# Performance work log

Hardware: AMD Instinct MI355X
Metric: run time of the kernel (lower is better)

Reference implementation:

```python
import jax, jax.numpy as jnp
import numpy as np

D_MODEL = 1024
NUM_HEADS = 16
HEAD_DIM = D_MODEL // NUM_HEADS  # 64
M_BITS = 32
B, N = 4, 2048


def setup_inputs() -> dict:
    key = jax.random.key(0)
    ks = jax.random.split(key, 6)
    s = 1.0 / np.sqrt(D_MODEL)
    se = 1.0 / np.sqrt(HEAD_DIM)
    return {
        "x": jax.random.normal(ks[0], (B, N, D_MODEL), dtype=jnp.float32),
        "Wq": jax.random.normal(ks[1], (D_MODEL, D_MODEL), dtype=jnp.float32) * s,
        "Wk": jax.random.normal(ks[2], (D_MODEL, D_MODEL), dtype=jnp.float32) * s,
        "Wv": jax.random.normal(ks[3], (D_MODEL, D_MODEL), dtype=jnp.float32) * s,
        # per-head witness (bit) encoders: project head_dim -> m_bits
        "W_enc": jax.random.normal(ks[4], (NUM_HEADS, HEAD_DIM, M_BITS), dtype=jnp.float32) * se,
        "Wo": jax.random.normal(ks[5], (D_MODEL, D_MODEL), dtype=jnp.float32) * s,
    }


def reference(x, Wq, Wk, Wv, W_enc, Wo):
    Bsz, Nq, _ = x.shape
    # QKV projections (nn.Linear, no bias): y = x @ W^T
    Q = x @ Wq.T
    K = x @ Wk.T  # self-attention: context = x
    V = x @ Wv.T
    # split heads: [B, N, H, hd]
    Qh = Q.reshape(Bsz, Nq, NUM_HEADS, HEAD_DIM)
    Kh = K.reshape(Bsz, Nq, NUM_HEADS, HEAD_DIM)
    Vh = V.reshape(Bsz, Nq, NUM_HEADS, HEAD_DIM)
    # witness encodings: soft-bit (tanh of random-hyperplane projections), m_bits << head_dim feature space
    q_enc = jnp.tanh(jnp.einsum("bnhd,hdm->bnhm", Qh, W_enc))
    k_enc = jnp.tanh(jnp.einsum("bnhd,hdm->bnhm", Kh, W_enc))
    # witness similarity scores over m_bits instead of full head_dim
    scale = 1.0 / np.sqrt(M_BITS)
    scores = jnp.einsum("bnhm,bkhm->bhnk", q_enc, k_enc) * scale  # [B,H,N,N]
    attn = jax.nn.softmax(scores, axis=-1)
    out = jnp.einsum("bhnk,bkhd->bnhd", attn, Vh).reshape(Bsz, Nq, D_MODEL)
    return out @ Wo.T
```

## Files before the change

### kernel.cpp

```cpp
#include <hip/hip_runtime.h>

typedef unsigned short u16;
typedef unsigned int u32;

typedef __bf16 bfrag __attribute__((ext_vector_type(8)));
typedef float f32x4 __attribute__((ext_vector_type(4)));

__device__ __forceinline__ float b2f(u16 h) {
    u32 u = ((u32)h) << 16;
    return __builtin_bit_cast(float, u);
}
__device__ __forceinline__ u16 f2b(float f) {
    u32 u = __builtin_bit_cast(u32, f);
    u += 0x7fffu + ((u >> 16) & 1u);
    return (u16)(u >> 16);
}
__device__ __forceinline__ u32 packt(float lo, float hi) {
    return (__builtin_bit_cast(u32, lo) >> 16) | (__builtin_bit_cast(u32, hi) & 0xffff0000u);
}

#if defined(__has_builtin)
#if __has_builtin(__builtin_amdgcn_exp2f)
#define EXP2(x) __builtin_amdgcn_exp2f(x)
#endif
#endif
#ifndef EXP2
#define EXP2(x) exp2f(x)
#endif

#if defined(__has_builtin)
#if __has_builtin(__builtin_amdgcn_global_load_lds)
#define HAS_GLL 1
#endif
#endif
#ifndef HAS_GLL
#define HAS_GLL 0
#endif

#if HAS_GLL
typedef __attribute__((address_space(1))) const u32 as1_u32;
typedef __attribute__((address_space(3))) u32 as3_u32;
__device__ __forceinline__ void gl_lds16(const u16* g, u16* l) {
    __builtin_amdgcn_global_load_lds((as1_u32*)g, (as3_u32*)l, 16, 0, 0);
}
#endif

#define BATCH 4
#define SEQ   2048
#define DM    1024
#define NH    16
#define HD    64
#define MB    32
#define STOK  (BATCH * SEQ)
#define QKVW  (3 * DM)

#define QSCALE 0.25503524337503433f
#define TWOLOG2E 2.8853900817779268f

__device__ __forceinline__ void storeC(u16* C, size_t idx, float v)   { C[idx] = f2b(v); }
__device__ __forceinline__ void storeC(float* C, size_t idx, float v) { C[idx] = v; }

__global__ __launch_bounds__(256) void cvt_f32_bf16(
    const float* __restrict__ s, u16* __restrict__ d, int n8)
{
    int i = blockIdx.x * 256 + threadIdx.x;
    if (i >= n8) return;
    const float4* sp = (const float4*)s + (size_t)i * 2;
    float4 a = sp[0], b = sp[1];
    u16 t[8] = { f2b(a.x), f2b(a.y), f2b(a.z), f2b(a.w),
                 f2b(b.x), f2b(b.y), f2b(b.z), f2b(b.w) };
    ((uint4*)d)[i] = *(uint4*)t;
}

__global__ __launch_bounds__(256) void cvt3_f32_bf16(
    const float* __restrict__ a, const float* __restrict__ b,
    const float* __restrict__ c, u16* __restrict__ d, int n8)
{
    const float* s = (blockIdx.y == 0) ? a : ((blockIdx.y == 1) ? b : c);
    u16* dd = d + (size_t)blockIdx.y * n8 * 8;
    int i = blockIdx.x * 256 + threadIdx.x;
    if (i >= n8) return;
    const float4* sp = (const float4*)s + (size_t)i * 2;
    float4 x = sp[0], y = sp[1];
    u16 t[8] = { f2b(x.x), f2b(x.y), f2b(x.z), f2b(x.w),
                 f2b(y.x), f2b(y.y), f2b(y.z), f2b(y.w) };
    ((uint4*)dd)[i] = *(uint4*)t;
}

template <int TBM, typename TC>
__global__ __launch_bounds__(256) void gemm_bt(
    const u16* __restrict__ A, const u16* __restrict__ Bt, TC* __restrict__ C,
    int M, int Nc, int K)
{
    constexpr int FI = TBM / 32;
    __shared__ alignas(16) u16 As[TBM * 32];
    __shared__ alignas(16) u16 Bs[128 * 32];

    const int tid  = threadIdx.x;
    const int wave = tid >> 6;
    const int lane = tid & 63;
    const int quad = lane >> 4;
    const int lrow = lane & 15;
    const int bm = blockIdx.y * TBM;
    const int bn = blockIdx.x * 128;
    const int wm = (wave & 1) * (TBM / 2);
    const int wn = (wave >> 1) * 64;

    f32x4 acc[FI][4] = {};

    for (int k0 = 0; k0 < K; k0 += 32) {
#if HAS_GLL
        for (int p = 0; p < TBM / 64; ++p) {
            int cbase = wave * TBM + p * 64;
            int cme   = cbase + lane;
            int row = cme >> 2, col = (cme & 3) * 8;
            gl_lds16(&A[(size_t)(bm + row) * K + k0 + col], &As[(size_t)cbase * 8]);
        }
        for (int p = 0; p < 2; ++p) {
            int cbase = wave * 128 + p * 64;
            int cme   = cbase + lane;
            int row = cme >> 2, col = (cme & 3) * 8;
            gl_lds16(&Bt[(size_t)(bn + row) * K + k0 + col], &Bs[(size_t)cbase * 8]);
        }
#else
        for (int p = 0; p < TBM / 64; ++p) {
            int idx = p * 256 + tid, row = idx >> 2, col = (idx & 3) * 8;
            *(uint4*)&As[row * 32 + col] = *(const uint4*)&A[(size_t)(bm + row) * K + k0 + col];
        }
        for (int p = 0; p < 2; ++p) {
            int idx = p * 256 + tid, row = idx >> 2, col = (idx & 3) * 8;
            *(uint4*)&Bs[row * 32 + col] = *(const uint4*)&Bt[(size_t)(bn + row) * K + k0 + col];
        }
#endif
        __syncthreads();

        bfrag af[FI], bfv[4];
        for (int i = 0; i < FI; ++i)
            af[i] = *(const bfrag*)&As[(wm + i * 16 + lrow) * 32 + quad * 8];
        for (int j = 0; j < 4; ++j)
            bfv[j] = *(const bfrag*)&Bs[(wn + j * 16 + lrow) * 32 + quad * 8];

        for (int i = 0; i < FI; ++i)
            for (int j = 0; j < 4; ++j)
                acc[i][j] = __builtin_amdgcn_mfma_f32_16x16x32_bf16(af[i], bfv[j], acc[i][j], 0, 0, 0);
        __syncthreads();
    }

    for (int i = 0; i < FI; ++i)
        for (int j = 0; j < 4; ++j)
            for (int r = 0; r < 4; ++r) {
                int row = bm + wm + i * 16 + quad * 4 + r;
                int col = bn + wn + j * 16 + lrow;
                storeC(C, (size_t)row * Nc + col, acc[i][j][r]);
            }
}

__global__ __launch_bounds__(256) void encode_mfma(
    const u16* __restrict__ QKV, const float* __restrict__ Wenc,
    u16* __restrict__ qe, u16* __restrict__ ke)
{
    const int nt = blockIdx.x;
    const int bh = blockIdx.y;
    const int b = bh >> 4, h = bh & 15;
    const int tid = threadIdx.x;
    const int wave = tid >> 6, lane = tid & 63, quad = lane >> 4, lrow = lane & 15;

    __shared__ alignas(16) u16 Wh[32 * 72];
    __shared__ alignas(16) u16 Wl[32 * 72];
    __shared__ alignas(16) u16 Xt[128 * 72];

    for (int p = 0; p < 8; ++p) {
        int d = p * 8 + (tid >> 5);
        int m = tid & 31;
        float w = Wenc[(size_t)h * (HD * MB) + d * MB + m];
        u16 hi = f2b(w);
        u16 lo = f2b(w - b2f(hi));
        Wh[m * 72 + d] = hi;
        Wl[m * 72 + d] = lo;
    }
    __syncthreads();

    bfrag bhf[2][2], blf[2][2];
    for (int n2 = 0; n2 < 2; ++n2)
        for (int kc = 0; kc < 2; ++kc) {
            bhf[n2][kc] = *(const bfrag*)&Wh[(n2 * 16 + lrow) * 72 + kc * 32 + quad * 8];
            blf[n2][kc] = *(const bfrag*)&Wl[(n2 * 16 + lrow) * 72 + kc * 32 + quad * 8];
        }

    const f32x4 zero = {0.f, 0.f, 0.f, 0.f};
    for (int src = 0; src < 2; ++src) {
        __syncthreads();
        const u16* base = QKV + (size_t)(b * SEQ + nt * 128) * QKVW + src * DM + h * HD;
        for (int p = 0; p < 4; ++p) {
            int idx = p * 256 + tid;
            int row = idx >> 3, cc = idx & 7;
            *(uint4*)&Xt[row * 72 + cc * 8] = *(const uint4*)&base[(size_t)row * QKVW + cc * 8];
        }
        __syncthreads();

        u16* dst = (src ? ke : qe) + ((size_t)bh * SEQ + (size_t)nt * 128) * MB;
        for (int i = 0; i < 2; ++i) {
            bfrag af[2];
            for (int kc = 0; kc < 2; ++kc)
                af[kc] = *(const bfrag*)&Xt[(wave * 32 + i * 16 + lrow) * 72 + kc * 32 + quad * 8];
            for (int n2 = 0; n2 < 2; ++n2) {
                f32x4 acc = zero;
                for (int kc = 0; kc < 2; ++kc) {
                    acc = __builtin_amdgcn_mfma_f32_16x16x32_bf16(af[kc], bhf[n2][kc], acc, 0, 0, 0);
                    acc = __builtin_amdgcn_mfma_f32_16x16x32_bf16(af[kc], blf[n2][kc], acc, 0, 0, 0);
                }
                for (int r = 0; r < 4; ++r) {
                    float e = EXP2(acc[r] * TWOLOG2E);
                    float t = 1.f - 2.f / (e + 1.f);
                    if (!src) t *= QSCALE;
                    int tok = wave * 32 + i * 16 + quad * 4 + r;
                    dst[(size_t)tok * MB + n2 * 16 + lrow] = f2b(t);
                }
            }
        }
    }
}

__global__ __launch_bounds__(256) void transpose_v(
    const u16* __restrict__ QKV, u16* __restrict__ Vt)
{
    const int nt = blockIdx.x, h = blockIdx.y, b = blockIdx.z;
    __shared__ alignas(16) u16 tile[64][72];
    const int tid = threadIdx.x;

    for (int p = 0; p < 2; ++p) {
        int idx = p * 256 + tid;
        int t  = idx >> 3;
        int dc = (idx & 7) * 8;
        *(uint4*)&tile[t][dc] =
            *(const uint4*)&QKV[(size_t)(b * SEQ + nt * 64 + t) * QKVW + 2 * DM + h * HD + dc];
    }
    __syncthreads();
    for (int p = 0; p < 2; ++p) {
        int idx = p * 256 + tid;
        int d  = idx >> 3;
        int tc = (idx & 7) * 8;
        u16 tmp[8];
        for (int j = 0; j < 8; ++j) tmp[j] = tile[tc + j][d];
        *(uint4*)&Vt[(size_t)((b * NH + h) * HD + d) * SEQ + nt * 64 + tc] = *(uint4*)tmp;
    }
}

__global__ __launch_bounds__(256) void flash_attn(
    const u16* __restrict__ qe,
    const u16* __restrict__ ke,
    const u16* __restrict__ Vt,
    u16* __restrict__ AO)
{
    const int h = blockIdx.x, b = blockIdx.y, qt = blockIdx.z;
    const int tid  = threadIdx.x;
    const int wave = tid >> 6;
    const int lane = tid & 63;
    const int quad = lane >> 4;
    const int lrow = lane & 15;

    __shared__ alignas(16) u16 Kt[2][64 * 32];
    __shared__ alignas(16) u16 Vtile[2][64 * 64];
    __shared__ alignas(16) u16 Plds[4][16 * 72];

    const size_t bhh = (size_t)(b * NH + h);
    const u16* keb = ke + bhh * SEQ * MB;
    const u16* qeb = qe + bhh * SEQ * MB;
    const u16* vtb = Vt + bhh * HD * SEQ;

    const int q0 = qt * 128 + wave * 32;

    const u16* ksrc = keb + tid * 8;
    const int d0 = wave * 8 + (lane >> 3);
    const int c0 = lane & 7;
    const int g0 = (c0 ^ (d0 & 7)) * 8;
    const u16* vsrc0 = vtb + (size_t)d0 * SEQ + g0;
    const u16* vsrc1 = vtb + (size_t)(d0 + 32) * SEQ + g0;

#if HAS_GLL
    gl_lds16(ksrc,  Kt[0] + wave * 512);
    gl_lds16(vsrc0, Vtile[0] + wave * 512);
    gl_lds16(vsrc1, Vtile[0] + 2048 + wave * 512);
#else
    *(uint4*)&Kt[0][tid * 8] = *(const uint4*)ksrc;
    *(uint4*)&Vtile[0][d0 * 64 + c0 * 8] = *(const uint4*)vsrc0;
    *(uint4*)&Vtile[0][(d0 + 32) * 64 + c0 * 8] = *(const uint4*)vsrc1;
#endif
    ksrc += 64 * MB;
    vsrc0 += 64;
    vsrc1 += 64;

    bfrag qf[2];
    for (int f = 0; f < 2; ++f)
        qf[f] = *(const bfrag*)&qeb[(size_t)(q0 + f * 16 + lrow) * MB + quad * 8];

    const bfrag ones = __builtin_bit_cast(bfrag,
        (uint4){0x3f803f80u, 0x3f803f80u, 0x3f803f80u, 0x3f803f80u});
    const f32x4 zero = {0.f, 0.f, 0.f, 0.f};

    f32x4 O[2][4] = {};
    f32x4 den[2] = {};
    const int sw = lrow & 7;

    for (int c = 0; c < 32; ++c) {
        const int cur = c & 1, nxt = cur ^ 1;
        __syncthreads();

        if (c + 1 < 32) {
#if HAS_GLL
            gl_lds16(ksrc,  Kt[nxt] + wave * 512);
            gl_lds16(vsrc0, Vtile[nxt] + wave * 512);
            gl_lds16(vsrc1, Vtile[nxt] + 2048 + wave * 512);
#else
            *(uint4*)&Kt[nxt][tid * 8] = *(const uint4*)ksrc;
            *(uint4*)&Vtile[nxt][d0 * 64 + c0 * 8] = *(const uint4*)vsrc0;
            *(uint4*)&Vtile[nxt][(d0 + 32) * 64 + c0 * 8] = *(const uint4*)vsrc1;
#endif
            ksrc += 64 * MB;
            vsrc0 += 64;
            vsrc1 += 64;
        }

        const u16* KtC = Kt[cur];
        const u16* VtC = Vtile[cur];

        bfrag kf[4];
        for (int t = 0; t < 4; ++t)
            kf[t] = *(const bfrag*)&KtC[(t * 16 + lrow) * 32 + quad * 8];

        bfrag pf[2][2];
        u16* P = Plds[wave];
        for (int f = 0; f < 2; ++f) {
            f32x4 St[4];
            __builtin_amdgcn_s_setprio(1);
            for (int t = 0; t < 4; ++t)
                St[t] = __builtin_amdgcn_mfma_f32_16x16x32_bf16(kf[t], qf[f], zero, 0, 0, 0);
            __builtin_amdgcn_s_setprio(0);
            for (int t = 0; t < 4; ++t) {
                float e0 = EXP2(St[t][0]);
                float e1 = EXP2(St[t][1]);
                float e2 = EXP2(St[t][2]);
                float e3 = EXP2(St[t][3]);
                uint2 pk = { packt(e0, e1), packt(e2, e3) };
                *(uint2*)&P[lrow * 72 + t * 16 + quad * 4] = pk;
            }
            for (int h2 = 0; h2 < 2; ++h2)
                pf[f][h2] = *(const bfrag*)&P[lrow * 72 + h2 * 32 + quad * 8];
        }

        __builtin_amdgcn_s_setprio(1);
        for (int f = 0; f < 2; ++f)
            for (int h2 = 0; h2 < 2; ++h2)
                den[f] = __builtin_amdgcn_mfma_f32_16x16x32_bf16(pf[f][h2], ones, den[f], 0, 0, 0);

        for (int j = 0; j < 4; ++j) {
            const u16* vrow = &VtC[(j * 16 + lrow) * 64];
            bfrag vf0 = *(const bfrag*)&vrow[((quad)     ^ sw) * 8];
            bfrag vf1 = *(const bfrag*)&vrow[((4 + quad) ^ sw) * 8];
            for (int f = 0; f < 2; ++f) {
                O[f][j] = __builtin_amdgcn_mfma_f32_16x16x32_bf16(pf[f][0], vf0, O[f][j], 0, 0, 0);
                O[f][j] = __builtin_amdgcn_mfma_f32_16x16x32_bf16(pf[f][1], vf1, O[f][j], 0, 0, 0);
            }
        }
        __builtin_amdgcn_s_setprio(0);
    }

    for (int f = 0; f < 2; ++f)
        for (int r = 0; r < 4; ++r) {
            float inv = 1.0f / den[f][r];
            size_t rowbase = (size_t)(b * SEQ + q0 + f * 16 + quad * 4 + r) * DM + h * HD;
            for (int j = 0; j < 4; ++j)
                AO[rowbase + j * 16 + lrow] = f2b(O[f][j][r] * inv);
        }
}

extern "C" void kernel_launch(void* const* d_in, const int* in_sizes, int n_in,
                              void* d_out, int out_size, void* d_ws, size_t ws_size,
                              hipStream_t stream) {
    const float* x    = (const float*)d_in[0];
    const float* Wq   = (const float*)d_in[1];
    const float* Wk   = (const float*)d_in[2];
    const float* Wv   = (const float*)d_in[3];
    const float* Wenc = (const float*)d_in[4];
    const float* Wo   = (const float*)d_in[5];
    float* out = (float*)d_out;

    const size_t MB1 = (size_t)1024 * 1024;
    char* ws = (char*)d_ws;
    u16* QKV = (u16*)(ws);
    u16* qe  = (u16*)(ws + 48 * MB1);
    u16* ke  = (u16*)(ws + 56 * MB1);
    u16* AO   = (u16*)(ws);
    u16* Wo_b = (u16*)(ws + 16 * MB1);

    u16* xb  = (u16*)d_out;
    u16* w3b = (u16*)((char*)d_out + 16 * MB1);
    u16* Vt  = (u16*)d_out;

    cvt_f32_bf16<<<dim3(STOK * DM / 8 / 256), 256, 0, stream>>>(x, xb, STOK * DM / 8);
    cvt3_f32_bf16<<<dim3(DM * DM / 8 / 256, 3), 256, 0, stream>>>(Wq, Wk, Wv, w3b, DM * DM / 8);

    gemm_bt<128, u16><<<dim3(QKVW / 128, STOK / 128), 256, 0, stream>>>(xb, w3b, QKV, STOK, QKVW, DM);

    encode_mfma<<<dim3(SEQ / 128, BATCH * NH), 256, 0, stream>>>(QKV, Wenc, qe, ke);
    transpose_v<<<dim3(SEQ / 64, NH, BATCH), 256, 0, stream>>>(QKV, Vt);
    cvt_f32_bf16<<<dim3(DM * DM / 8 / 256), 256, 0, stream>>>(Wo, Wo_b, DM * DM / 8);

    flash_attn<<<dim3(NH, BATCH, SEQ / 128), 256, 0, stream>>>(qe, ke, Vt, AO);

    gemm_bt<64, float><<<dim3(DM / 128, STOK / 64), 256, 0, stream>>>(AO, Wo_b, out, STOK, DM, DM);
}
```

Measured before the change: 296.4 us.

## Switch flash attention to 32x32x16 MFMA with register-resident P via permlane swap

```diff
diff --git a/kernel.cpp b/kernel.cpp
--- a/kernel.cpp
+++ b/kernel.cpp
@@ -5,6 +5,7 @@
 
 typedef __bf16 bfrag __attribute__((ext_vector_type(8)));
 typedef float f32x4 __attribute__((ext_vector_type(4)));
+typedef float f32x16 __attribute__((ext_vector_type(16)));
 
 __device__ __forceinline__ float b2f(u16 h) {
     u32 u = ((u32)h) << 16;
@@ -44,6 +45,30 @@
     __builtin_amdgcn_global_load_lds((as1_u32*)g, (as3_u32*)l, 16, 0, 0);
 }
 #endif
+
+#if defined(__has_builtin)
+#if __has_builtin(__builtin_amdgcn_permlane32_swap)
+#define HAS_PLS 1
+#endif
+#endif
+#ifndef HAS_PLS
+#define HAS_PLS 0
+#endif
+
+__device__ __forceinline__ void plswap(u32 a, u32 b, u32& o0, u32& o1) {
+#if HAS_PLS
+    auto r = __builtin_amdgcn_permlane32_swap((int)a, (int)b, false, false);
+    o0 = (u32)r[0];
+    o1 = (u32)r[1];
+#else
+    int idx = ((int)(threadIdx.x & 63) ^ 32) << 2;
+    u32 ca = (u32)__builtin_amdgcn_ds_bpermute(idx, (int)a);
+    u32 cb = (u32)__builtin_amdgcn_ds_bpermute(idx, (int)b);
+    bool hi = (threadIdx.x & 63) >= 32;
+    o0 = hi ? cb : a;
+    o1 = hi ? b : ca;
+#endif
+}
 
 #define BATCH 4
 #define SEQ   2048
@@ -246,7 +271,7 @@
     }
 }
 
-__global__ __launch_bounds__(256) void flash_attn(
+__global__ __launch_bounds__(256, 3) void flash_attn(
     const u16* __restrict__ qe,
     const u16* __restrict__ ke,
     const u16* __restrict__ Vt,
@@ -256,21 +281,22 @@
     const int tid  = threadIdx.x;
     const int wave = tid >> 6;
     const int lane = tid & 63;
-    const int quad = lane >> 4;
-    const int lrow = lane & 15;
+    const int r31  = lane & 31;
+    const int hi   = lane >> 5;
 
     __shared__ alignas(16) u16 Kt[2][64 * 32];
     __shared__ alignas(16) u16 Vtile[2][64 * 64];
-    __shared__ alignas(16) u16 Plds[4][16 * 72];
 
     const size_t bhh = (size_t)(b * NH + h);
     const u16* keb = ke + bhh * SEQ * MB;
     const u16* qeb = qe + bhh * SEQ * MB;
     const u16* vtb = Vt + bhh * HD * SEQ;
 
-    const int q0 = qt * 128 + wave * 32;
-
-    const u16* ksrc = keb + tid * 8;
+    const int q0w = qt * 128 + wave * 32;
+
+    const int klr = tid >> 2;
+    const int ksl = tid & 3;
+    const u16* ksrc = keb + (size_t)klr * MB + ((ksl ^ (klr & 3)) * 8);
     const int d0 = wave * 8 + (lane >> 3);
     const int c0 = lane & 7;
     const int g0 = (c0 ^ (d0 & 7)) * 8;
@@ -282,7 +308,7 @@
     gl_lds16(vsrc0, Vtile[0] + wave * 512);
     gl_lds16(vsrc1, Vtile[0] + 2048 + wave * 512);
 #else
-    *(uint4*)&Kt[0][tid * 8] = *(const uint4*)ksrc;
+    *(uint4*)&Kt[0][klr * 32 + ksl * 8] = *(const uint4*)ksrc;
     *(uint4*)&Vtile[0][d0 * 64 + c0 * 8] = *(const uint4*)vsrc0;
     *(uint4*)&Vtile[0][(d0 + 32) * 64 + c0 * 8] = *(const uint4*)vsrc1;
 #endif
@@ -291,16 +317,20 @@
     vsrc1 += 64;
 
     bfrag qf[2];
-    for (int f = 0; f < 2; ++f)
-        qf[f] = *(const bfrag*)&qeb[(size_t)(q0 + f * 16 + lrow) * MB + quad * 8];
+    {
+        const u16* qrow = qeb + (size_t)(q0w + r31) * MB;
+        qf[0] = *(const bfrag*)&qrow[hi * 8];
+        qf[1] = *(const bfrag*)&qrow[16 + hi * 8];
+    }
 
     const bfrag ones = __builtin_bit_cast(bfrag,
         (uint4){0x3f803f80u, 0x3f803f80u, 0x3f803f80u, 0x3f803f80u});
-    const f32x4 zero = {0.f, 0.f, 0.f, 0.f};
-
-    f32x4 O[2][4] = {};
-    f32x4 den[2] = {};
-    const int sw = lrow & 7;
+    const f32x16 zero16 = {};
+
+    f32x16 Oa[2] = {};
+    f32x16 den32 = {};
+    const int ksw = r31 & 3;
+    const int vsw = r31 & 7;
 
     for (int c = 0; c < 32; ++c) {
         const int cur = c & 1, nxt = cur ^ 1;
@@ -312,7 +342,7 @@
             gl_lds16(vsrc0, Vtile[nxt] + wave * 512);
             gl_lds16(vsrc1, Vtile[nxt] + 2048 + wave * 512);
 #else
-            *(uint4*)&Kt[nxt][tid * 8] = *(const uint4*)ksrc;
+            *(uint4*)&Kt[nxt][klr * 32 + ksl * 8] = *(const uint4*)ksrc;
             *(uint4*)&Vtile[nxt][d0 * 64 + c0 * 8] = *(const uint4*)vsrc0;
             *(uint4*)&Vtile[nxt][(d0 + 32) * 64 + c0 * 8] = *(const uint4*)vsrc1;
 #endif
@@ -324,54 +354,66 @@
         const u16* KtC = Kt[cur];
         const u16* VtC = Vtile[cur];
 
-        bfrag kf[4];
-        for (int t = 0; t < 4; ++t)
-            kf[t] = *(const bfrag*)&KtC[(t * 16 + lrow) * 32 + quad * 8];
+        bfrag kf[2][2];
+        for (int kt = 0; kt < 2; ++kt) {
+            const u16* krow = &KtC[(kt * 32 + r31) * 32];
+            kf[kt][0] = *(const bfrag*)&krow[((hi    ) ^ ksw) * 8];
+            kf[kt][1] = *(const bfrag*)&krow[((2 + hi) ^ ksw) * 8];
+        }
 
         bfrag pf[2][2];
-        u16* P = Plds[wave];
-        for (int f = 0; f < 2; ++f) {
-            f32x4 St[4];
+        for (int kt = 0; kt < 2; ++kt) {
             __builtin_amdgcn_s_setprio(1);
-            for (int t = 0; t < 4; ++t)
-                St[t] = __builtin_amdgcn_mfma_f32_16x16x32_bf16(kf[t], qf[f], zero, 0, 0, 0);
+            f32x16 St = __builtin_amdgcn_mfma_f32_32x32x16_bf16(kf[kt][0], qf[0], zero16, 0, 0, 0);
+            St = __builtin_amdgcn_mfma_f32_32x32x16_bf16(kf[kt][1], qf[1], St, 0, 0, 0);
             __builtin_amdgcn_s_setprio(0);
-            for (int t = 0; t < 4; ++t) {
-                float e0 = EXP2(St[t][0]);
-                float e1 = EXP2(St[t][1]);
-                float e2 = EXP2(St[t][2]);
-                float e3 = EXP2(St[t][3]);
-                uint2 pk = { packt(e0, e1), packt(e2, e3) };
-                *(uint2*)&P[lrow * 72 + t * 16 + quad * 4] = pk;
+            for (int kc = 0; kc < 2; ++kc) {
+                float e0 = EXP2(St[8 * kc + 0]);
+                float e1 = EXP2(St[8 * kc + 1]);
+                float e2 = EXP2(St[8 * kc + 2]);
+                float e3 = EXP2(St[8 * kc + 3]);
+                float e4 = EXP2(St[8 * kc + 4]);
+                float e5 = EXP2(St[8 * kc + 5]);
+                float e6 = EXP2(St[8 * kc + 6]);
+                float e7 = EXP2(St[8 * kc + 7]);
+                u32 A0 = packt(e0, e1), A1 = packt(e2, e3);
+                u32 B0 = packt(e4, e5), B1 = packt(e6, e7);
+                u32 w0, w1, w2, w3;
+                plswap(A0, B0, w0, w2);
+                plswap(A1, B1, w1, w3);
+                uint4 words = { w0, w1, w2, w3 };
+                pf[kt][kc] = __builtin_bit_cast(bfrag, words);
             }
-            for (int h2 = 0; h2 < 2; ++h2)
-                pf[f][h2] = *(const bfrag*)&P[lrow * 72 + h2 * 32 + quad * 8];
         }
 
         __builtin_amdgcn_s_setprio(1);
-        for (int f = 0; f < 2; ++f)
-            for (int h2 = 0; h2 < 2; ++h2)
-                den[f] = __builtin_amdgcn_mfma_f32_16x16x32_bf16(pf[f][h2], ones, den[f], 0, 0, 0);
-
-        for (int j = 0; j < 4; ++j) {
-            const u16* vrow = &VtC[(j * 16 + lrow) * 64];
-            bfrag vf0 = *(const bfrag*)&vrow[((quad)     ^ sw) * 8];
-            bfrag vf1 = *(const bfrag*)&vrow[((4 + quad) ^ sw) * 8];
-            for (int f = 0; f < 2; ++f) {
-                O[f][j] = __builtin_amdgcn_mfma_f32_16x16x32_bf16(pf[f][0], vf0, O[f][j], 0, 0, 0);
-                O[f][j] = __builtin_amdgcn_mfma_f32_16x16x32_bf16(pf[f][1], vf1, O[f][j], 0, 0, 0);
+        for (int kt = 0; kt < 2; ++kt)
+            for (int kc = 0; kc < 2; ++kc)
+                den32 = __builtin_amdgcn_mfma_f32_32x32x16_bf16(ones, pf[kt][kc], den32, 0, 0, 0);
+
+        for (int dt = 0; dt < 2; ++dt) {
+            const u16* vrow = &VtC[(dt * 32 + r31) * 64];
+            for (int kt = 0; kt < 2; ++kt)
+                for (int kc = 0; kc < 2; ++kc) {
+                    bfrag vf = *(const bfrag*)&vrow[(((kt * 4 + kc * 2 + hi) ^ vsw) * 8)];
+                    Oa[dt] = __builtin_amdgcn_mfma_f32_32x32x16_bf16(vf, pf[kt][kc], Oa[dt], 0, 0, 0);
+                }
+        }
+        __builtin_amdgcn_s_setprio(0);
+    }
+
+    {
+        float inv = 1.0f / den32[0];
+        u16* aob = AO + (size_t)(b * SEQ + q0w + r31) * DM + h * HD;
+        for (int dt = 0; dt < 2; ++dt)
+            for (int g = 0; g < 4; ++g) {
+                u16 t4[4] = { f2b(Oa[dt][g * 4 + 0] * inv),
+                              f2b(Oa[dt][g * 4 + 1] * inv),
+                              f2b(Oa[dt][g * 4 + 2] * inv),
+                              f2b(Oa[dt][g * 4 + 3] * inv) };
+                *(uint2*)&aob[dt * 32 + g * 8 + hi * 4] = *(uint2*)t4;
             }
-        }
-        __builtin_amdgcn_s_setprio(0);
-    }
-
-    for (int f = 0; f < 2; ++f)
-        for (int r = 0; r < 4; ++r) {
-            float inv = 1.0f / den[f][r];
-            size_t rowbase = (size_t)(b * SEQ + q0 + f * 16 + quad * 4 + r) * DM + h * HD;
-            for (int j = 0; j < 4; ++j)
-                AO[rowbase + j * 16 + lrow] = f2b(O[f][j][r] * inv);
-        }
+    }
 }
 
 extern "C" void kernel_launch(void* const* d_in, const int* in_sizes, int n_in,
```

Result: no change. 298.7 us (+0.8%).
